# Kernel tuning notes

Hardware: AMD Instinct MI355X
Metric: run time of the kernel (lower is better)

Reference implementation:

```python
import jax, jax.numpy as jnp
import numpy as np

N, E, B = 100000, 1600000, 512
NE, EE, H = 32, 32, 64
SCALE = float(2**48 - 1)


def _mlp2(x, W1, b1, W2, b2):
    # Linear -> ReLU -> Linear
    return jax.nn.relu(x @ W1 + b1) @ W2 + b2


def _gine(x, src, dst, e, W1, b1, W2, b2, n):
    # GINEConv (eps=0): nn(x + sum_j relu(x_j + e_ij))
    m = jax.nn.relu(x[src] + e)                      # [E, d] gather + edge add
    agg = jax.ops.segment_sum(m, dst, num_segments=n)  # scatter-add to targets
    return _mlp2(x + agg, W1, b1, W2, b2)


def _encode(names, edge_index, edge_attr, batch,
            idW1, idb1, idW2, idb2, edW1, edb1, edW2, edb2,
            c1W1, c1b1, c1W2, c1b2, c2W1, c2b1, c2W2, c2b2, linW, linb):
    norm = jnp.clip((names.astype(jnp.float32) + 2.0) / SCALE, 0.0, 1.0)[:, None]
    x = _mlp2(norm, idW1, idb1, idW2, idb2)          # [N, NE]
    e = _mlp2(edge_attr, edW1, edb1, edW2, edb2)     # [E, EE]
    src, dst = edge_index[0], edge_index[1]
    x = jax.nn.relu(_gine(x, src, dst, e, c1W1, c1b1, c1W2, c1b2, N))
    e2 = e @ linW + linb                             # edge lin for conv2 (EE->H)
    x = jax.nn.relu(_gine(x, src, dst, e2, c2W1, c2b1, c2W2, c2b2, N))
    sums = jax.ops.segment_sum(x, batch, num_segments=B)
    cnt = jax.ops.segment_sum(jnp.ones((x.shape[0],), x.dtype), batch, num_segments=B)
    return sums / jnp.maximum(cnt, 1.0)[:, None]     # global_mean_pool


def setup_inputs() -> dict:
    key = jax.random.key(0)
    ks = iter(jax.random.split(key, 64))
    def w(shape):
        return jax.random.normal(next(ks), shape, dtype=jnp.float32) * 0.05
    d = {}
    d['node_names_s'] = jax.random.randint(next(ks), (N,), 0, 1000000)
    d['edge_index_s'] = jax.random.randint(next(ks), (2, E), 0, N)
    d['edge_attr_s'] = jax.random.uniform(next(ks), (E, 1), dtype=jnp.float32)
    d['batch_s'] = jnp.sort(jax.random.randint(next(ks), (N,), 0, B))
    d['node_names_g'] = jax.random.randint(next(ks), (N,), 0, 1000000)
    d['edge_index_g'] = jax.random.randint(next(ks), (2, E), 0, N)
    d['edge_attr_g'] = jax.random.uniform(next(ks), (E, 1), dtype=jnp.float32)
    d['batch_g'] = jnp.sort(jax.random.randint(next(ks), (N,), 0, B))
    d['depth'] = jax.random.uniform(next(ks), (B,), dtype=jnp.float32)
    # shared encoders
    d['idW1'], d['idb1'], d['idW2'], d['idb2'] = w((1, NE)), w((NE,)), w((NE, NE)), w((NE,))
    d['edW1'], d['edb1'], d['edW2'], d['edb2'] = w((1, EE)), w((EE,)), w((EE, EE)), w((EE,))
    # state convs
    d['s1W1'], d['s1b1'], d['s1W2'], d['s1b2'] = w((NE, H)), w((H,)), w((H, H)), w((H,))
    d['s2W1'], d['s2b1'], d['s2W2'], d['s2b2'] = w((H, H)), w((H,)), w((H, H)), w((H,))
    d['s2linW'], d['s2linb'] = w((EE, H)), w((H,))
    # goal convs
    d['g1W1'], d['g1b1'], d['g1W2'], d['g1b2'] = w((NE, H)), w((H,)), w((H, H)), w((H,))
    d['g2W1'], d['g2b1'], d['g2W2'], d['g2b2'] = w((H, H)), w((H,)), w((H, H)), w((H,))
    d['g2linW'], d['g2linb'] = w((EE, H)), w((H,))
    d['rW1'], d['rb1'], d['rW2'], d['rb2'] = w((2 * H + 1, H)), w((H,)), w((H, 1)), w((1,))
    return d


def reference(node_names_s, edge_index_s, edge_attr_s, batch_s,
              node_names_g, edge_index_g, edge_attr_g, batch_g, depth,
              idW1, idb1, idW2, idb2, edW1, edb1, edW2, edb2,
              s1W1, s1b1, s1W2, s1b2, s2W1, s2b1, s2W2, s2b2, s2linW, s2linb,
              g1W1, g1b1, g1W2, g1b2, g2W1, g2b1, g2W2, g2b2, g2linW, g2linb,
              rW1, rb1, rW2, rb2):
    s = _encode(node_names_s, edge_index_s, edge_attr_s, batch_s,
                idW1, idb1, idW2, idb2, edW1, edb1, edW2, edb2,
                s1W1, s1b1, s1W2, s1b2, s2W1, s2b1, s2W2, s2b2, s2linW, s2linb)
    g = _encode(node_names_g, edge_index_g, edge_attr_g, batch_g,
                idW1, idb1, idW2, idb2, edW1, edb1, edW2, edb2,
                g1W1, g1b1, g1W2, g1b2, g2W1, g2b1, g2W2, g2b2, g2linW, g2linb)
    z = jnp.concatenate([s, g, depth[:, None]], axis=1)  # [B, 2H+1]
    return _mlp2(z, rW1, rb1, rW2, rb2)[:, 0]            # [B]
```

## Files before the change

kernel.cpp:

```cpp
#include <hip/hip_runtime.h>
#include <hip/hip_fp16.h>
#include <stdint.h>

namespace {

constexpr int NN   = 100000;
constexpr int TN   = 2 * NN;
constexpr int NEDG = 1600000;
constexpr int TE   = 2 * NEDG;
constexpr int NBAT = 512;
constexpr int NSEG = 33;

constexpr int NC     = 782;
constexpr int TILE   = 4096;
constexpr int ABLK   = (TE + TILE - 1) / TILE;
constexpr int ENTCAP = 5120;

constexpr int CONVBLK = 2048;

constexpr int S1H = 20;
constexpr int S2H = 36;

constexpr int TAB_BP = 0;
constexpr int TAB_D1 = 32;
// ... 103 lines not shown
    if (t < 32) bp[t] = tabs[TAB_BP + t];
    for (int i = t; i < NC; i += 256) hist[i] = 0;
    __syncthreads();
    int base = blockIdx.x * TILE;
#pragma unroll
    for (int j = 0; j < 16; ++j) {
      int i = base + j * 256 + t;
      if (i < TE) {
        int d = (i < NEDG) ? dst_s[i] : (dst_g[i - NEDG] + NN);
        atomicAdd(&hist[d >> 8], 1);
      }
    }
    __syncthreads();
    int loc[4];
    int sum = 0;
#pragma unroll
    for (int j = 0; j < 4; ++j) {
      int b = t * 4 + j;
      int v = (b < NC) ? hist[b] : 0;
      loc[j] = sum; sum += v;
    }
    scanbuf[t] = sum;
    __syncthreads();
    for (int st = 1; st < 256; st <<= 1) {
      int u = (t >= st) ? scanbuf[t - st] : 0;
      __syncthreads();
      scanbuf[t] += u;
      __syncthreads();
    }
    int texcl = scanbuf[t] - sum;
#pragma unroll
    for (int j = 0; j < 4; ++j) {
      int b = t * 4 + j;
      if (b < NC) { lofs[b] = texcl + loc[j]; lcur[b] = 0; }
    }
    __syncthreads();
    for (int b = t; b < NC; b += 256) {
      int c = hist[b];
      hist[b] = c ? atomicAdd(&gcur[b], c) : 0;
    }
    __syncthreads();
#pragma unroll
    for (int j = 0; j < 16; ++j) {
      int i = base + j * 256 + t;
      if (i < TE) {
        int sl, d; float a;
        if (i < NEDG) { sl = src_s[i]; d = dst_s[i]; a = attr_s[i]; }
        else { int k = i - NEDG; sl = src_g[k]; d = dst_g[k] + NN; a = attr_g[k]; }
        int seg = 0;
#pragma unroll
        for (int q = 0; q < 32; ++q) seg += (bp[q] < a);
        int c = d >> 8;
        int r = atomicAdd(&lcur[c], 1);
        int s = lofs[c] + r;
        sorted[s] = make_int2(sl | ((d & 255) << 17) | (seg << 25), __float_as_int(a));
        addr[s] = c * ENTCAP + hist[c] + r;
      }
    }
    __syncthreads();
    int tot = (base + TILE <= TE) ? TILE : (TE - base);
    for (int s = t; s < tot; s += 256) part[addr[s]] = sorted[s];
  } else if (blockIdx.x < ABLK + 782) {
    int n = (blockIdx.x - ABLK) * 256 + t;
    if (n >= TN) return;
    int name = (n < NN) ? names_s[n] : names_g[n - NN];
    float norm = ((float)name + 2.0f) / 281474976710655.0f;
    norm = fminf(fmaxf(norm, 0.0f), 1.0f);
    float h[32];
#pragma unroll
    for (int i = 0; i < 32; ++i) h[i] = relu_(fmaf(norm, idW1[i], idb1[i]));
    int2* outh = (int2*)(x0h + (size_t)n * 32);
    for (int j0 = 0; j0 < 32; j0 += 4) {
      float a0 = idb2[j0], a1 = idb2[j0 + 1], a2 = idb2[j0 + 2], a3 = idb2[j0 + 3];
#pragma unroll
      for (int i = 0; i < 32; ++i) {
        float hv = h[i];
        a0 = fmaf(hv, idW2[i * 32 + j0],     a0);
        a1 = fmaf(hv, idW2[i * 32 + j0 + 1], a1);
        a2 = fmaf(hv, idW2[i * 32 + j0 + 2], a2);
        a3 = fmaf(hv, idW2[i * 32 + j0 + 3], a3);
      }
      outh[j0 >> 2] = make_int2(f2h2(a0, a1), f2h2(a2, a3));
    }
  } else {
    int blk = blockIdx.x - ABLK - 782;
    int half = blk >= 391;
    const int* bat = half ? bat_g : bat_s;
    int* start = half ? start_g : start_s;
    int i = (blk - half * 391) * 256 + t;
    if (i >= NN) return;
    int cur = bat[i];
    int prev = (i == 0) ? -1 : bat[i - 1];
    for (int b = prev + 1; b <= cur; ++b) start[b] = i;
    if (i == NN - 1) {
      for (int b = cur + 1; b <= NBAT; ++b) start[b] = NN;
    }
  }
}

__global__ __launch_bounds__(1024) void coarse_scan(
    const int* __restrict__ gcur, int* __restrict__ cbase, int* __restrict__ rowptr) {
  __shared__ int s[1024];
  int t = threadIdx.x;
  int v = (t < NC) ? min(gcur[t], ENTCAP) : 0;
  s[t] = v;
  __syncthreads();
  for (int st = 1; st < 1024; st <<= 1) {
    int u = (t >= st) ? s[t - st] : 0;
    __syncthreads();
    s[t] += u;
    __syncthreads();
  }
  if (t < NC) cbase[t] = s[t] - v;
  if (t == 0) rowptr[TN] = TE;
}

__global__ __launch_bounds__(256) void partition_to_csr(
    const int* __restrict__ gcur, const int* __restrict__ cbase,
    const int2* __restrict__ part,
    int* __restrict__ rowptr, int2* __restrict__ colattr) {
  __shared__ int2 outE[ENTCAP];
  __shared__ int hist[256];
  __shared__ int cur[256];
  __shared__ int sc[256];
  int t = threadIdx.x, b = blockIdx.x;
  hist[t] = 0;
  __syncthreads();
  int cnt = min(gcur[b], ENTCAP);
  int ibase = b * ENTCAP;
  int obase = cbase[b];
  for (int i = t; i < cnt; i += 256)
    atomicAdd(&hist[(part[ibase + i].x >> 17) & 255], 1);
  __syncthreads();
  int v = hist[t];
  sc[t] = v;
  __syncthreads();
  for (int st = 1; st < 256; st <<= 1) {
    int u = (t >= st) ? sc[t - st] : 0;
    __syncthreads();
    sc[t] += u;
    __syncthreads();
  }
  int excl = sc[t] - v;
  int gnode = b * 256 + t;
  if (gnode < TN) rowptr[gnode] = obase + excl;
  cur[t] = excl;
  __syncthreads();
  for (int i = t; i < cnt; i += 256) {
    int2 e = part[ibase + i];
    int dl = (e.x >> 17) & 255;
    int srcn = e.x & 0x1FFFF;
    int seg = (e.x >> 25) & 63;
    int pos = atomicAdd(&cur[dl], 1);
    outE[pos] = make_int2(srcn | (seg << 20), e.y);
  }
  __syncthreads();
  for (int i = t; i < cnt; i += 256) colattr[obase + i] = outE[i];
}

__global__ __launch_bounds__(256) void conv1_dual(
    const __half* __restrict__ x0h,
    const int* __restrict__ rowptr, const int2* __restrict__ colattr,
    const float* __restrict__ tabs, float* __restrict__ hb) {
  __shared__ __half2 dt2[NSEG * S1H];
  __shared__ __half2 ct2[NSEG * S1H];
  for (int i = threadIdx.x; i < NSEG * 16; i += 256) {
    int s = i >> 4, j = i & 15;
    dt2[s * S1H + j] = __floats2half2_rn(tabs[TAB_D1 + s * 32 + 2 * j],
                                         tabs[TAB_D1 + s * 32 + 2 * j + 1]);
    ct2[s * S1H + j] = __floats2half2_rn(tabs[TAB_C1 + s * 32 + 2 * j],
                                         tabs[TAB_C1 + s * 32 + 2 * j + 1]);
  }
  __syncthreads();
  int lane = threadIdx.x & 63;
  int sub = lane & 7;
  int f0  = (lane >> 3) * 4;
  int h0  = (lane >> 3) * 2;
  int wid = blockIdx.x * 4 + (threadIdx.x >> 6);
  int nb = rowptr[wid], ne = rowptr[wid + 1];
  for (int n = wid; n < TN; n += 4 * CONVBLK) {
    int beg = nb, end = ne;
    int n2 = n + 4 * CONVBLK;
    if (n2 < TN) { nb = rowptr[n2]; ne = rowptr[n2 + 1]; }
    const __half* xb = x0h + (n >= NN ? (size_t)NN * 32 : 0);
    int2 sv = make_int2(0, 0);
    if (sub == 0) sv = *(const int2*)(x0h + (size_t)n * 32 + f0);
    float4 acc = make_float4(0.f, 0.f, 0.f, 0.f);
    for (int k = beg + sub; k < end; k += 16) {
      int2 ca0 = colattr[k];
      int kb = k + 8;
      bool has1 = kb < end;
      int2 ca1 = has1 ? colattr[kb] : ca0;
      unsigned p0 = (unsigned)ca0.x, p1 = (unsigned)ca1.x;
      int s0 = (int)(p0 & 0xFFFFFu), g0 = (int)(p0 >> 20);
      int s1 = (int)(p1 & 0xFFFFFu), g1 = (int)(p1 >> 20);
      float a0 = __int_as_float(ca0.y), a1 = __int_as_float(ca1.y);
      __half2 az0 = __floats2half2_rn(a0, a0);
      __half2 az1 = __floats2half2_rn(a1, a1);
      int2 xv0 = *(const int2*)(xb + (size_t)s0 * 32 + f0);
      int2 xv1 = *(const int2*)(xb + (size_t)s1 * 32 + f0);
      int2 dv0 = *(const int2*)&dt2[g0 * S1H + h0];
      int2 cv0 = *(const int2*)&ct2[g0 * S1H + h0];
      __half2 v;
      float2 f;
      v = __hadd2(bch(xv0.x), __hfma2(az0, bch(dv0.x), bch(cv0.x)));
      f = __half22float2(v); acc.x += relu_(f.x); acc.y += relu_(f.y);
      v = __hadd2(bch(xv0.y), __hfma2(az0, bch(dv0.y), bch(cv0.y)));
      f = __half22float2(v); acc.z += relu_(f.x); acc.w += relu_(f.y);
      if (has1) {
        int2 dv1 = *(const int2*)&dt2[g1 * S1H + h0];
        int2 cv1 = *(const int2*)&ct2[g1 * S1H + h0];
        v = __hadd2(bch(xv1.x), __hfma2(az1, bch(dv1.x), bch(cv1.x)));
        f = __half22float2(v); acc.x += relu_(f.x); acc.y += relu_(f.y);
        v = __hadd2(bch(xv1.y), __hfma2(az1, bch(dv1.y), bch(cv1.y)));
        f = __half22float2(v); acc.z += relu_(f.x); acc.w += relu_(f.y);
      }
    }
#pragma unroll
    for (int m = 1; m < 8; m <<= 1) {
      float4 o = shfl_xor4(acc, m);
      acc.x += o.x; acc.y += o.y; acc.z += o.z; acc.w += o.w;
    }
    if (sub == 0) {
      float2 t0 = __half22float2(bch(sv.x)), t1 = __half22float2(bch(sv.y));
      *(float4*)(hb + (size_t)n * 32 + f0) =
          make_float4(t0.x + acc.x, t0.y + acc.y, t1.x + acc.z, t1.y + acc.w);
    }
  }
}

__global__ __launch_bounds__(256) void conv2_dual(
    const __half* __restrict__ x1h,
    const int* __restrict__ rowptr, const int2* __restrict__ colattr,
    const float* __restrict__ tabs, float* __restrict__ hb) {
  __shared__ __half2 dt2[NSEG * S2H];
  __shared__ __half2 ct2[NSEG * S2H];
  int halfg = blockIdx.x >= (CONVBLK / 2);
  const float* d2 = tabs + TAB_E2 + (size_t)halfg * 2 * NSEG * 64;
  for (int i = threadIdx.x; i < NSEG * 32; i += 256) {
    int s = i >> 5, j = i & 31;
    dt2[s * S2H + j] = __floats2half2_rn(d2[s * 64 + 2 * j], d2[s * 64 + 2 * j + 1]);
    ct2[s * S2H + j] = __floats2half2_rn(d2[NSEG * 64 + s * 64 + 2 * j],
                                         d2[NSEG * 64 + s * 64 + 2 * j + 1]);
  }
  __syncthreads();
  const __half* xb = x1h + (size_t)halfg * NN * 64;
  int lane = threadIdx.x & 63;
  int sub = lane & 7;
  int f0  = (lane >> 3) * 8;
  int h0  = (lane >> 3) * 4;
  int wid = (blockIdx.x - halfg * (CONVBLK / 2)) * 4 + (threadIdx.x >> 6);
  int nlim = halfg * NN + NN;
  int n0 = halfg * NN + wid;
  int nb = rowptr[n0], ne = rowptr[n0 + 1];
  for (int n = n0; n < nlim; n += 2 * CONVBLK) {
    int beg = nb, end = ne;
    int n2 = n + 2 * CONVBLK;
    if (n2 < nlim) { nb = rowptr[n2]; ne = rowptr[n2 + 1]; }
    int4 sv0 = make_int4(0, 0, 0, 0);
    if (sub == 0) sv0 = *(const int4*)(x1h + (size_t)n * 64 + f0);
    float4 accA = make_float4(0.f, 0.f, 0.f, 0.f);
    float4 accB = make_float4(0.f, 0.f, 0.f, 0.f);
    for (int k = beg + sub; k < end; k += 16) {
      int2 ca0 = colattr[k];
      int kb = k + 8;
      bool has1 = kb < end;
      int2 ca1 = has1 ? colattr[kb] : ca0;
      unsigned p0 = (unsigned)ca0.x, p1 = (unsigned)ca1.x;
      int s0 = (int)(p0 & 0xFFFFFu), g0 = (int)(p0 >> 20);
      int s1 = (int)(p1 & 0xFFFFFu), g1 = (int)(p1 >> 20);
      float a0 = __int_as_float(ca0.y), a1 = __int_as_float(ca1.y);
      __half2 az0 = __floats2half2_rn(a0, a0);
      __half2 az1 = __floats2half2_rn(a1, a1);
      int4 xv0 = *(const int4*)(xb + (size_t)s0 * 64 + f0);
      int4 xv1 = *(const int4*)(xb + (size_t)s1 * 64 + f0);
      int4 dv0 = *(const int4*)&dt2[g0 * S2H + h0];
      int4 cv0 = *(const int4*)&ct2[g0 * S2H + h0];
      __half2 v;
      float2 f;
      v = __hadd2(bch(xv0.x), __hfma2(az0, bch(dv0.x), bch(cv0.x)));
      f = __half22float2(v); accA.x += relu_(f.x); accA.y += relu_(f.y);
      v = __hadd2(bch(xv0.y), __hfma2(az0, bch(dv0.y), bch(cv0.y)));
      f = __half22float2(v); accA.z += relu_(f.x); accA.w += relu_(f.y);
      v = __hadd2(bch(xv0.z), __hfma2(az0, bch(dv0.z), bch(cv0.z)));
      f = __half22float2(v); accB.x += relu_(f.x); accB.y += relu_(f.y);
      v = __hadd2(bch(xv0.w), __hfma2(az0, bch(dv0.w), bch(cv0.w)));
      f = __half22float2(v); accB.z += relu_(f.x); accB.w += relu_(f.y);
      if (has1) {
        int4 dv1 = *(const int4*)&dt2[g1 * S2H + h0];
        int4 cv1 = *(const int4*)&ct2[g1 * S2H + h0];
        v = __hadd2(bch(xv1.x), __hfma2(az1, bch(dv1.x), bch(cv1.x)));
        f = __half22float2(v); accA.x += relu_(f.x); accA.y += relu_(f.y);
        v = __hadd2(bch(xv1.y), __hfma2(az1, bch(dv1.y), bch(cv1.y)));
        f = __half22float2(v); accA.z += relu_(f.x); accA.w += relu_(f.y);
        v = __hadd2(bch(xv1.z), __hfma2(az1, bch(dv1.z), bch(cv1.z)));
        f = __half22float2(v); accB.x += relu_(f.x); accB.y += relu_(f.y);
        v = __hadd2(bch(xv1.w), __hfma2(az1, bch(dv1.w), bch(cv1.w)));
        f = __half22float2(v); accB.z += relu_(f.x); accB.w += relu_(f.y);
      }
    }
#pragma unroll
    for (int m = 1; m < 8; m <<= 1) {
      float4 oA = shfl_xor4(accA, m);
      float4 oB = shfl_xor4(accB, m);
      accA.x += oA.x; accA.y += oA.y; accA.z += oA.z; accA.w += oA.w;
      accB.x += oB.x; accB.y += oB.y; accB.z += oB.z; accB.w += oB.w;
    }
    if (sub == 0) {
      float2 t0 = __half22float2(bch(sv0.x)), t1 = __half22float2(bch(sv0.y));
      float2 t2 = __half22float2(bch(sv0.z)), t3 = __half22float2(bch(sv0.w));
      float* op = hb + (size_t)n * 64 + f0;
      *(float4*)op       = make_float4(t0.x + accA.x, t0.y + accA.y, t1.x + accA.z, t1.y + accA.w);
      *(float4*)(op + 4) = make_float4(t2.x + accB.x, t2.y + accB.y, t3.x + accB.z, t3.y + accB.w);
    }
  }
}

__global__ __launch_bounds__(256) void mlp1_dual(
    const float* __restrict__ hin,
    const float* __restrict__ sW1, const float* __restrict__ sb1,
    const float* __restrict__ sW2, const float* __restrict__ sb2,
    const float* __restrict__ gW1, const float* __restrict__ gb1,
    const float* __restrict__ gW2, const float* __restrict__ gb2,
    __half* __restrict__ hout) {
  constexpr int IN = 32;
  __shared__ float hsT[IN][65];
  __shared__ float ysT[64][65];
  int base = blockIdx.x * 64;
  for (int idx = threadIdx.x; idx < 64 * IN; idx += 256) {
    int node = idx / IN, k = idx - node * IN;
    hsT[k][node] = hin[(size_t)(base + node) * IN + k];
  }
  __syncthreads();
  int nt = threadIdx.x >> 4, jx = threadIdx.x & 15;
  int n0 = nt * 4, f0 = jx * 4;
  bool isg = (base + n0) >= NN;
  const float* W1 = isg ? gW1 : sW1;
  const float* b1 = isg ? gb1 : sb1;
  const float* W2 = isg ? gW2 : sW2;
  const float* b2 = isg ? gb2 : sb2;
  float4 acc0, acc1, acc2, acc3;
  {
    const float4 b = *(const float4*)(b1 + f0);
    acc0 = b; acc1 = b; acc2 = b; acc3 = b;
  }
  for (int k = 0; k < IN; ++k) {
    const float4 h = *(const float4*)&hsT[k][n0];
    const float4 w = *(const float4*)(W1 + k * 64 + f0);
    acc0.x = fmaf(h.x, w.x, acc0.x); acc0.y = fmaf(h.x, w.y, acc0.y);
    acc0.z = fmaf(h.x, w.z, acc0.z); acc0.w = fmaf(h.x, w.w, acc0.w);
    acc1.x = fmaf(h.y, w.x, acc1.x); acc1.y = fmaf(h.y, w.y, acc1.y);
    acc1.z = fmaf(h.y, w.z, acc1.z); acc1.w = fmaf(h.y, w.w, acc1.w);
    acc2.x = fmaf(h.z, w.x, acc2.x); acc2.y = fmaf(h.z, w.y, acc2.y);
    acc2.z = fmaf(h.z, w.z, acc2.z); acc2.w = fmaf(h.z, w.w, acc2.w);
    acc3.x = fmaf(h.w, w.x, acc3.x); acc3.y = fmaf(h.w, w.y, acc3.y);
    acc3.z = fmaf(h.w, w.z, acc3.z); acc3.w = fmaf(h.w, w.w, acc3.w);
  }
  ysT[f0 + 0][n0 + 0] = relu_(acc0.x); ysT[f0 + 1][n0 + 0] = relu_(acc0.y);
  ysT[f0 + 2][n0 + 0] = relu_(acc0.z); ysT[f0 + 3][n0 + 0] = relu_(acc0.w);
  ysT[f0 + 0][n0 + 1] = relu_(acc1.x); ysT[f0 + 1][n0 + 1] = relu_(acc1.y);
  ysT[f0 + 2][n0 + 1] = relu_(acc1.z); ysT[f0 + 3][n0 + 1] = relu_(acc1.w);
  ysT[f0 + 0][n0 + 2] = relu_(acc2.x); ysT[f0 + 1][n0 + 2] = relu_(acc2.y);
  ysT[f0 + 2][n0 + 2] = relu_(acc2.z); ysT[f0 + 3][n0 + 2] = relu_(acc2.w);
  ysT[f0 + 0][n0 + 3] = relu_(acc3.x); ysT[f0 + 1][n0 + 3] = relu_(acc3.y);
  ysT[f0 + 2][n0 + 3] = relu_(acc3.z); ysT[f0 + 3][n0 + 3] = relu_(acc3.w);
  __syncthreads();
  {
    const float4 b = *(const float4*)(b2 + f0);
    acc0 = b; acc1 = b; acc2 = b; acc3 = b;
  }
  for (int k = 0; k < 64; ++k) {
    const float4 h = *(const float4*)&ysT[k][n0];
    const float4 w = *(const float4*)(W2 + k * 64 + f0);
    acc0.x = fmaf(h.x, w.x, acc0.x); acc0.y = fmaf(h.x, w.y, acc0.y);
    acc0.z = fmaf(h.x, w.z, acc0.z); acc0.w = fmaf(h.x, w.w, acc0.w);
    acc1.x = fmaf(h.y, w.x, acc1.x); acc1.y = fmaf(h.y, w.y, acc1.y);
    acc1.z = fmaf(h.y, w.z, acc1.z); acc1.w = fmaf(h.y, w.w, acc1.w);
    acc2.x = fmaf(h.z, w.x, acc2.x); acc2.y = fmaf(h.z, w.y, acc2.y);
    acc2.z = fmaf(h.z, w.z, acc2.z); acc2.w = fmaf(h.z, w.w, acc2.w);
    acc3.x = fmaf(h.w, w.x, acc3.x); acc3.y = fmaf(h.w, w.y, acc3.y);
    acc3.z = fmaf(h.w, w.z, acc3.z); acc3.w = fmaf(h.w, w.w, acc3.w);
  }
  float4 o;
  o = make_float4(relu_(acc0.x), relu_(acc0.y), relu_(acc0.z), relu_(acc0.w));
  *(int2*)(hout + (size_t)(base + n0 + 0) * 64 + f0) = make_int2(f2h2(o.x, o.y), f2h2(o.z, o.w));
  o = make_float4(relu_(acc1.x), relu_(acc1.y), relu_(acc1.z), relu_(acc1.w));
  *(int2*)(hout + (size_t)(base + n0 + 1) * 64 + f0) = make_int2(f2h2(o.x, o.y), f2h2(o.z, o.w));
  o = make_float4(relu_(acc2.x), relu_(acc2.y), relu_(acc2.z), relu_(acc2.w));
  *(int2*)(hout + (size_t)(base + n0 + 2) * 64 + f0) = make_int2(f2h2(o.x, o.y), f2h2(o.z, o.w));
  o = make_float4(relu_(acc3.x), relu_(acc3.y), relu_(acc3.z), relu_(acc3.w));
  *(int2*)(hout + (size_t)(base + n0 + 3) * 64 + f0) = make_int2(f2h2(o.x, o.y), f2h2(o.z, o.w));
}

__global__ __launch_bounds__(256) void mlp2_pool_dual(
    const float* __restrict__ hin,
    const float* __restrict__ sW1, const float* __restrict__ sb1,
    const float* __restrict__ sW2, const float* __restrict__ sb2,
    const float* __restrict__ gW1, const float* __restrict__ gb1,
    const float* __restrict__ gW2, const float* __restrict__ gb2,
    const int* __restrict__ bat_s, const int* __restrict__ bat_g,
    float* __restrict__ psum) {
  constexpr int IN = 64;
  __shared__ float hsT[IN][65];
  __shared__ float ysT[64][65];
  __shared__ int pid[64];
  int base = blockIdx.x * 64;
  for (int idx = threadIdx.x; idx < 64 * IN; idx += 256) {
    int node = idx / IN, k = idx - node * IN;
    hsT[k][node] = hin[(size_t)(base + node) * IN + k];
  }
  if (threadIdx.x < 64) {
    int gb = base + threadIdx.x;
    pid[threadIdx.x] = (gb < NN) ? bat_s[gb] : (NBAT + bat_g[gb - NN]);
  }
  __syncthreads();
  int nt = threadIdx.x >> 4, jx = threadIdx.x & 15;
  int n0 = nt * 4, f0 = jx * 4;
  bool isg = (base + n0) >= NN;
  const float* W1 = isg ? gW1 : sW1;
  const float* b1 = isg ? gb1 : sb1;
  const float* W2 = isg ? gW2 : sW2;
  const float* b2 = isg ? gb2 : sb2;
  float4 acc0, acc1, acc2, acc3;
  {
    const float4 b = *(const float4*)(b1 + f0);
    acc0 = b; acc1 = b; acc2 = b; acc3 = b;
  }
  for (int k = 0; k < IN; ++k) {
    const float4 h = *(const float4*)&hsT[k][n0];
    const float4 w = *(const float4*)(W1 + k * 64 + f0);
    acc0.x = fmaf(h.x, w.x, acc0.x); acc0.y = fmaf(h.x, w.y, acc0.y);
    acc0.z = fmaf(h.x, w.z, acc0.z); acc0.w = fmaf(h.x, w.w, acc0.w);
    acc1.x = fmaf(h.y, w.x, acc1.x); acc1.y = fmaf(h.y, w.y, acc1.y);
    acc1.z = fmaf(h.y, w.z, acc1.z); acc1.w = fmaf(h.y, w.w, acc1.w);
    acc2.x = fmaf(h.z, w.x, acc2.x); acc2.y = fmaf(h.z, w.y, acc2.y);
    acc2.z = fmaf(h.z, w.z, acc2.z); acc2.w = fmaf(h.z, w.w, acc2.w);
    acc3.x = fmaf(h.w, w.x, acc3.x); acc3.y = fmaf(h.w, w.y, acc3.y);
    acc3.z = fmaf(h.w, w.z, acc3.z); acc3.w = fmaf(h.w, w.w, acc3.w);
  }
  ysT[f0 + 0][n0 + 0] = relu_(acc0.x); ysT[f0 + 1][n0 + 0] = relu_(acc0.y);
  ysT[f0 + 2][n0 + 0] = relu_(acc0.z); ysT[f0 + 3][n0 + 0] = relu_(acc0.w);
  ysT[f0 + 0][n0 + 1] = relu_(acc1.x); ysT[f0 + 1][n0 + 1] = relu_(acc1.y);
  ysT[f0 + 2][n0 + 1] = relu_(acc1.z); ysT[f0 + 3][n0 + 1] = relu_(acc1.w);
  ysT[f0 + 0][n0 + 2] = relu_(acc2.x); ysT[f0 + 1][n0 + 2] = relu_(acc2.y);
  ysT[f0 + 2][n0 + 2] = relu_(acc2.z); ysT[f0 + 3][n0 + 2] = relu_(acc2.w);
  ysT[f0 + 0][n0 + 3] = relu_(acc3.x); ysT[f0 + 1][n0 + 3] = relu_(acc3.y);
  ysT[f0 + 2][n0 + 3] = relu_(acc3.z); ysT[f0 + 3][n0 + 3] = relu_(acc3.w);
  __syncthreads();
  {
    const float4 b = *(const float4*)(b2 + f0);
    acc0 = b; acc1 = b; acc2 = b; acc3 = b;
  }
  for (int k = 0; k < 64; ++k) {
    const float4 h = *(const float4*)&ysT[k][n0];
    const float4 w = *(const float4*)(W2 + k * 64 + f0);
    acc0.x = fmaf(h.x, w.x, acc0.x); acc0.y = fmaf(h.x, w.y, acc0.y);
    acc0.z = fmaf(h.x, w.z, acc0.z); acc0.w = fmaf(h.x, w.w, acc0.w);
    acc1.x = fmaf(h.y, w.x, acc1.x); acc1.y = fmaf(h.y, w.y, acc1.y);
    acc1.z = fmaf(h.y, w.z, acc1.z); acc1.w = fmaf(h.y, w.w, acc1.w);
    acc2.x = fmaf(h.z, w.x, acc2.x); acc2.y = fmaf(h.z, w.y, acc2.y);
    acc2.z = fmaf(h.z, w.z, acc2.z); acc2.w = fmaf(h.z, w.w, acc2.w);
    acc3.x = fmaf(h.w, w.x, acc3.x); acc3.y = fmaf(h.w, w.y, acc3.y);
    acc3.z = fmaf(h.w, w.z, acc3.z); acc3.w = fmaf(h.w, w.w, acc3.w);
  }
  __syncthreads();
  ysT[f0 + 0][n0 + 0] = relu_(acc0.x); ysT[f0 + 1][n0 + 0] = relu_(acc0.y);
  ysT[f0 + 2][n0 + 0] = relu_(acc0.z); ysT[f0 + 3][n0 + 0] = relu_(acc0.w);
// ... 147 lines not shown
```

Baseline: 569.7 us.

## Process two nodes per wave with masked branchless edge loops in GINE convs

Each wave in conv1 and conv2 now handles two destination nodes at a time. A single masked, branch-free loop issues four colattr loads and four gathered x loads per iteration, which raises memory-level parallelism for the latency-bound gathers. Out-of-range lanes use clamped indices with a zero multiplier instead of a branch. The CSR build also pre-converts the edge attribute to a packed half2, removing a conversion per edge. The cost is extra register pressure and wasted loads when the two nodes have unequal degrees.

```diff
diff --git a/kernel.cpp b/kernel.cpp
--- a/kernel.cpp
+++ b/kernel.cpp
@@ -279,10 +279,23 @@
     int srcn = e.x & 0x1FFFF;
     int seg = (e.x >> 25) & 63;
     int pos = atomicAdd(&cur[dl], 1);
-    outE[pos] = make_int2(srcn | (seg << 20), e.y);
+    float af = __int_as_float(e.y);
+    outE[pos] = make_int2(srcn | (seg << 20), f2h2(af, af));
   }
   __syncthreads();
   for (int i = t; i < cnt; i += 256) colattr[obase + i] = outE[i];
+}
+
+__device__ __forceinline__ void e1m(int2 xv, unsigned p, int h0, __half2 az, float m,
+                                    const __half2* dt2, const __half2* ct2, float4& A) {
+  int g = (int)(p >> 20);
+  int2 dv = *(const int2*)&dt2[g * S1H + h0];
+  int2 cv = *(const int2*)&ct2[g * S1H + h0];
+  __half2 v; float2 f;
+  v = __hadd2(bch(xv.x), __hfma2(az, bch(dv.x), bch(cv.x)));
+  f = __half22float2(v); A.x = fmaf(m, relu_(f.x), A.x); A.y = fmaf(m, relu_(f.y), A.y);
+  v = __hadd2(bch(xv.y), __hfma2(az, bch(dv.y), bch(cv.y)));
+  f = __half22float2(v); A.z = fmaf(m, relu_(f.x), A.z); A.w = fmaf(m, relu_(f.y), A.w);
 }
 
 __global__ __launch_bounds__(256) void conv1_dual(
@@ -303,57 +316,87 @@
   int sub = lane & 7;
   int f0  = (lane >> 3) * 4;
   int h0  = (lane >> 3) * 2;
+  constexpr int STR = 4 * CONVBLK;
   int wid = blockIdx.x * 4 + (threadIdx.x >> 6);
-  int nb = rowptr[wid], ne = rowptr[wid + 1];
-  for (int n = wid; n < TN; n += 4 * CONVBLK) {
-    int beg = nb, end = ne;
-    int n2 = n + 4 * CONVBLK;
-    if (n2 < TN) { nb = rowptr[n2]; ne = rowptr[n2 + 1]; }
-    const __half* xb = x0h + (n >= NN ? (size_t)NN * 32 : 0);
-    int2 sv = make_int2(0, 0);
-    if (sub == 0) sv = *(const int2*)(x0h + (size_t)n * 32 + f0);
-    float4 acc = make_float4(0.f, 0.f, 0.f, 0.f);
-    for (int k = beg + sub; k < end; k += 16) {
-      int2 ca0 = colattr[k];
-      int kb = k + 8;
-      bool has1 = kb < end;
-      int2 ca1 = has1 ? colattr[kb] : ca0;
-      unsigned p0 = (unsigned)ca0.x, p1 = (unsigned)ca1.x;
-      int s0 = (int)(p0 & 0xFFFFFu), g0 = (int)(p0 >> 20);
-      int s1 = (int)(p1 & 0xFFFFFu), g1 = (int)(p1 >> 20);
-      float a0 = __int_as_float(ca0.y), a1 = __int_as_float(ca1.y);
-      __half2 az0 = __floats2half2_rn(a0, a0);
-      __half2 az1 = __floats2half2_rn(a1, a1);
-      int2 xv0 = *(const int2*)(xb + (size_t)s0 * 32 + f0);
-      int2 xv1 = *(const int2*)(xb + (size_t)s1 * 32 + f0);
-      int2 dv0 = *(const int2*)&dt2[g0 * S1H + h0];
-      int2 cv0 = *(const int2*)&ct2[g0 * S1H + h0];
-      __half2 v;
-      float2 f;
-      v = __hadd2(bch(xv0.x), __hfma2(az0, bch(dv0.x), bch(cv0.x)));
-      f = __half22float2(v); acc.x += relu_(f.x); acc.y += relu_(f.y);
-      v = __hadd2(bch(xv0.y), __hfma2(az0, bch(dv0.y), bch(cv0.y)));
-      f = __half22float2(v); acc.z += relu_(f.x); acc.w += relu_(f.y);
-      if (has1) {
-        int2 dv1 = *(const int2*)&dt2[g1 * S1H + h0];
-        int2 cv1 = *(const int2*)&ct2[g1 * S1H + h0];
-        v = __hadd2(bch(xv1.x), __hfma2(az1, bch(dv1.x), bch(cv1.x)));
-        f = __half22float2(v); acc.x += relu_(f.x); acc.y += relu_(f.y);
-        v = __hadd2(bch(xv1.y), __hfma2(az1, bch(dv1.y), bch(cv1.y)));
-        f = __half22float2(v); acc.z += relu_(f.x); acc.w += relu_(f.y);
+  int nbA = rowptr[wid], neA = rowptr[wid + 1];
+  int nbB = 0, neB = 0;
+  if (wid + STR < TN) { nbB = rowptr[wid + STR]; neB = rowptr[wid + STR + 1]; }
+  for (int n = wid; n < TN; n += 2 * STR) {
+    int nB = n + STR;
+    bool hasB = nB < TN;
+    int begA = nbA, endA = neA, begB = nbB, endB = neB;
+    int nn = n + 2 * STR;
+    if (nn < TN) {
+      nbA = rowptr[nn]; neA = rowptr[nn + 1];
+      if (nn + STR < TN) { nbB = rowptr[nn + STR]; neB = rowptr[nn + STR + 1]; }
+      else { nbB = 0; neB = 0; }
+    }
+    const __half* xbA = x0h + (n  >= NN ? (size_t)NN * 32 : 0);
+    const __half* xbB = x0h + (nB >= NN ? (size_t)NN * 32 : 0);
+    float4 accA = make_float4(0.f, 0.f, 0.f, 0.f);
+    float4 accB = make_float4(0.f, 0.f, 0.f, 0.f);
+    int kA = begA + sub, kB = begB + sub;
+    while (__any((kA < endA) || (kB < endB))) {
+      int iA0 = min(kA, TE - 1), iA1 = min(kA + 8, TE - 1);
+      int iB0 = min(kB, TE - 1), iB1 = min(kB + 8, TE - 1);
+      float mA0 = (kA < endA)     ? 1.f : 0.f;
+      float mA1 = (kA + 8 < endA) ? 1.f : 0.f;
+      float mB0 = (kB < endB)     ? 1.f : 0.f;
+      float mB1 = (kB + 8 < endB) ? 1.f : 0.f;
+      int2 cA0 = colattr[iA0], cA1 = colattr[iA1];
+      int2 cB0 = colattr[iB0], cB1 = colattr[iB1];
+      unsigned pA0 = (unsigned)cA0.x, pA1 = (unsigned)cA1.x;
+      unsigned pB0 = (unsigned)cB0.x, pB1 = (unsigned)cB1.x;
+      int2 xA0 = *(const int2*)(xbA + (size_t)(pA0 & 0xFFFFFu) * 32 + f0);
+      int2 xA1 = *(const int2*)(xbA + (size_t)(pA1 & 0xFFFFFu) * 32 + f0);
+      int2 xB0 = *(const int2*)(xbB + (size_t)(pB0 & 0xFFFFFu) * 32 + f0);
+      int2 xB1 = *(const int2*)(xbB + (size_t)(pB1 & 0xFFFFFu) * 32 + f0);
+      e1m(xA0, pA0, h0, bch(cA0.y), mA0, dt2, ct2, accA);
+      e1m(xA1, pA1, h0, bch(cA1.y), mA1, dt2, ct2, accA);
+      e1m(xB0, pB0, h0, bch(cB0.y), mB0, dt2, ct2, accB);
+      e1m(xB1, pB1, h0, bch(cB1.y), mB1, dt2, ct2, accB);
+      kA += 16; kB += 16;
+    }
+    int2 svA = make_int2(0, 0), svB = make_int2(0, 0);
+    if (sub == 0) {
+      svA = *(const int2*)(x0h + (size_t)n * 32 + f0);
+      if (hasB) svB = *(const int2*)(x0h + (size_t)nB * 32 + f0);
+    }
+#pragma unroll
+    for (int m = 1; m < 8; m <<= 1) {
+      float4 oA = shfl_xor4(accA, m);
+      float4 oB = shfl_xor4(accB, m);
+      accA.x += oA.x; accA.y += oA.y; accA.z += oA.z; accA.w += oA.w;
+      accB.x += oB.x; accB.y += oB.y; accB.z += oB.z; accB.w += oB.w;
+    }
+    if (sub == 0) {
+      float2 t0 = __half22float2(bch(svA.x)), t1 = __half22float2(bch(svA.y));
+      *(float4*)(hb + (size_t)n * 32 + f0) =
+          make_float4(t0.x + accA.x, t0.y + accA.y, t1.x + accA.z, t1.y + accA.w);
+      if (hasB) {
+        float2 u0 = __half22float2(bch(svB.x)), u1 = __half22float2(bch(svB.y));
+        *(float4*)(hb + (size_t)nB * 32 + f0) =
+            make_float4(u0.x + accB.x, u0.y + accB.y, u1.x + accB.z, u1.y + accB.w);
       }
     }
-#pragma unroll
-    for (int m = 1; m < 8; m <<= 1) {
-      float4 o = shfl_xor4(acc, m);
-      acc.x += o.x; acc.y += o.y; acc.z += o.z; acc.w += o.w;
-    }
-    if (sub == 0) {
-      float2 t0 = __half22float2(bch(sv.x)), t1 = __half22float2(bch(sv.y));
-      *(float4*)(hb + (size_t)n * 32 + f0) =
-          make_float4(t0.x + acc.x, t0.y + acc.y, t1.x + acc.z, t1.y + acc.w);
-    }
-  }
+  }
+}
+
+__device__ __forceinline__ void e2m(int4 xv, unsigned p, int h0, __half2 az, float m,
+                                    const __half2* dt2, const __half2* ct2,
+                                    float4& A, float4& B) {
+  int g = (int)(p >> 20);
+  int4 dv = *(const int4*)&dt2[g * S2H + h0];
+  int4 cv = *(const int4*)&ct2[g * S2H + h0];
+  __half2 v; float2 f;
+  v = __hadd2(bch(xv.x), __hfma2(az, bch(dv.x), bch(cv.x)));
+  f = __half22float2(v); A.x = fmaf(m, relu_(f.x), A.x); A.y = fmaf(m, relu_(f.y), A.y);
+  v = __hadd2(bch(xv.y), __hfma2(az, bch(dv.y), bch(cv.y)));
+  f = __half22float2(v); A.z = fmaf(m, relu_(f.x), A.z); A.w = fmaf(m, relu_(f.y), A.w);
+  v = __hadd2(bch(xv.z), __hfma2(az, bch(dv.z), bch(cv.z)));
+  f = __half22float2(v); B.x = fmaf(m, relu_(f.x), B.x); B.y = fmaf(m, relu_(f.y), B.y);
+  v = __hadd2(bch(xv.w), __hfma2(az, bch(dv.w), bch(cv.w)));
+  f = __half22float2(v); B.z = fmaf(m, relu_(f.x), B.z); B.w = fmaf(m, relu_(f.y), B.w);
 }
 
 __global__ __launch_bounds__(256) void conv2_dual(
@@ -376,69 +419,78 @@
   int sub = lane & 7;
   int f0  = (lane >> 3) * 8;
   int h0  = (lane >> 3) * 4;
+  constexpr int STR2 = 2 * CONVBLK;
   int wid = (blockIdx.x - halfg * (CONVBLK / 2)) * 4 + (threadIdx.x >> 6);
   int nlim = halfg * NN + NN;
   int n0 = halfg * NN + wid;
-  int nb = rowptr[n0], ne = rowptr[n0 + 1];
-  for (int n = n0; n < nlim; n += 2 * CONVBLK) {
-    int beg = nb, end = ne;
-    int n2 = n + 2 * CONVBLK;
-    if (n2 < nlim) { nb = rowptr[n2]; ne = rowptr[n2 + 1]; }
-    int4 sv0 = make_int4(0, 0, 0, 0);
-    if (sub == 0) sv0 = *(const int4*)(x1h + (size_t)n * 64 + f0);
-    float4 accA = make_float4(0.f, 0.f, 0.f, 0.f);
-    float4 accB = make_float4(0.f, 0.f, 0.f, 0.f);
-    for (int k = beg + sub; k < end; k += 16) {
-      int2 ca0 = colattr[k];
-      int kb = k + 8;
-      bool has1 = kb < end;
-      int2 ca1 = has1 ? colattr[kb] : ca0;
-      unsigned p0 = (unsigned)ca0.x, p1 = (unsigned)ca1.x;
-      int s0 = (int)(p0 & 0xFFFFFu), g0 = (int)(p0 >> 20);
-      int s1 = (int)(p1 & 0xFFFFFu), g1 = (int)(p1 >> 20);
-      float a0 = __int_as_float(ca0.y), a1 = __int_as_float(ca1.y);
-      __half2 az0 = __floats2half2_rn(a0, a0);
-      __half2 az1 = __floats2half2_rn(a1, a1);
-      int4 xv0 = *(const int4*)(xb + (size_t)s0 * 64 + f0);
-      int4 xv1 = *(const int4*)(xb + (size_t)s1 * 64 + f0);
-      int4 dv0 = *(const int4*)&dt2[g0 * S2H + h0];
-      int4 cv0 = *(const int4*)&ct2[g0 * S2H + h0];
-      __half2 v;
-      float2 f;
-      v = __hadd2(bch(xv0.x), __hfma2(az0, bch(dv0.x), bch(cv0.x)));
-      f = __half22float2(v); accA.x += relu_(f.x); accA.y += relu_(f.y);
-      v = __hadd2(bch(xv0.y), __hfma2(az0, bch(dv0.y), bch(cv0.y)));
-      f = __half22float2(v); accA.z += relu_(f.x); accA.w += relu_(f.y);
-      v = __hadd2(bch(xv0.z), __hfma2(az0, bch(dv0.z), bch(cv0.z)));
-      f = __half22float2(v); accB.x += relu_(f.x); accB.y += relu_(f.y);
-      v = __hadd2(bch(xv0.w), __hfma2(az0, bch(dv0.w), bch(cv0.w)));
-      f = __half22float2(v); accB.z += relu_(f.x); accB.w += relu_(f.y);
-      if (has1) {
-        int4 dv1 = *(const int4*)&dt2[g1 * S2H + h0];
-        int4 cv1 = *(const int4*)&ct2[g1 * S2H + h0];
-        v = __hadd2(bch(xv1.x), __hfma2(az1, bch(dv1.x), bch(cv1.x)));
-        f = __half22float2(v); accA.x += relu_(f.x); accA.y += relu_(f.y);
-        v = __hadd2(bch(xv1.y), __hfma2(az1, bch(dv1.y), bch(cv1.y)));
-        f = __half22float2(v); accA.z += relu_(f.x); accA.w += relu_(f.y);
-        v = __hadd2(bch(xv1.z), __hfma2(az1, bch(dv1.z), bch(cv1.z)));
-        f = __half22float2(v); accB.x += relu_(f.x); accB.y += relu_(f.y);
-        v = __hadd2(bch(xv1.w), __hfma2(az1, bch(dv1.w), bch(cv1.w)));
-        f = __half22float2(v); accB.z += relu_(f.x); accB.w += relu_(f.y);
+  int nbA = rowptr[n0], neA = rowptr[n0 + 1];
+  int nbB = 0, neB = 0;
+  if (n0 + STR2 < nlim) { nbB = rowptr[n0 + STR2]; neB = rowptr[n0 + STR2 + 1]; }
+  for (int n = n0; n < nlim; n += 2 * STR2) {
+    int nB = n + STR2;
+    bool hasB = nB < nlim;
+    int begA = nbA, endA = neA, begB = nbB, endB = neB;
+    int nn = n + 2 * STR2;
+    if (nn < nlim) {
+      nbA = rowptr[nn]; neA = rowptr[nn + 1];
+      if (nn + STR2 < nlim) { nbB = rowptr[nn + STR2]; neB = rowptr[nn + STR2 + 1]; }
+      else { nbB = 0; neB = 0; }
+    }
+    float4 accA0 = make_float4(0.f, 0.f, 0.f, 0.f);
+    float4 accA1 = make_float4(0.f, 0.f, 0.f, 0.f);
+    float4 accB0 = make_float4(0.f, 0.f, 0.f, 0.f);
+    float4 accB1 = make_float4(0.f, 0.f, 0.f, 0.f);
+    int kA = begA + sub, kB = begB + sub;
+    while (__any((kA < endA) || (kB < endB))) {
+      int iA0 = min(kA, TE - 1), iA1 = min(kA + 8, TE - 1);
+      int iB0 = min(kB, TE - 1), iB1 = min(kB + 8, TE - 1);
+      float mA0 = (kA < endA)     ? 1.f : 0.f;
+      float mA1 = (kA + 8 < endA) ? 1.f : 0.f;
+      float mB0 = (kB < endB)     ? 1.f : 0.f;
+      float mB1 = (kB + 8 < endB) ? 1.f : 0.f;
+      int2 cA0 = colattr[iA0], cA1 = colattr[iA1];
+      int2 cB0 = colattr[iB0], cB1 = colattr[iB1];
+      unsigned pA0 = (unsigned)cA0.x, pA1 = (unsigned)cA1.x;
+      unsigned pB0 = (unsigned)cB0.x, pB1 = (unsigned)cB1.x;
+      int4 xA0 = *(const int4*)(xb + (size_t)(pA0 & 0xFFFFFu) * 64 + f0);
+      int4 xA1 = *(const int4*)(xb + (size_t)(pA1 & 0xFFFFFu) * 64 + f0);
+      int4 xB0 = *(const int4*)(xb + (size_t)(pB0 & 0xFFFFFu) * 64 + f0);
+      int4 xB1 = *(const int4*)(xb + (size_t)(pB1 & 0xFFFFFu) * 64 + f0);
+      e2m(xA0, pA0, h0, bch(cA0.y), mA0, dt2, ct2, accA0, accA1);
+      e2m(xA1, pA1, h0, bch(cA1.y), mA1, dt2, ct2, accA0, accA1);
+      e2m(xB0, pB0, h0, bch(cB0.y), mB0, dt2, ct2, accB0, accB1);
+      e2m(xB1, pB1, h0, bch(cB1.y), mB1, dt2, ct2, accB0, accB1);
+      kA += 16; kB += 16;
+    }
+    int4 svA = make_int4(0, 0, 0, 0), svB = make_int4(0, 0, 0, 0);
+    if (sub == 0) {
+      svA = *(const int4*)(x1h + (size_t)n * 64 + f0);
+      if (hasB) svB = *(const int4*)(x1h + (size_t)nB * 64 + f0);
+    }
+#pragma unroll
+    for (int m = 1; m < 8; m <<= 1) {
+      float4 o0 = shfl_xor4(accA0, m);
+      float4 o1 = shfl_xor4(accA1, m);
+      float4 o2 = shfl_xor4(accB0, m);
+      float4 o3 = shfl_xor4(accB1, m);
+      accA0.x += o0.x; accA0.y += o0.y; accA0.z += o0.z; accA0.w += o0.w;
+      accA1.x += o1.x; accA1.y += o1.y; accA1.z += o1.z; accA1.w += o1.w;
+      accB0.x += o2.x; accB0.y += o2.y; accB0.z += o2.z; accB0.w += o2.w;
+      accB1.x += o3.x; accB1.y += o3.y; accB1.z += o3.z; accB1.w += o3.w;
+    }
+    if (sub == 0) {
+      float2 t0 = __half22float2(bch(svA.x)), t1 = __half22float2(bch(svA.y));
+      float2 t2 = __half22float2(bch(svA.z)), t3 = __half22float2(bch(svA.w));
+      float* op = hb + (size_t)n * 64 + f0;
+      *(float4*)op       = make_float4(t0.x + accA0.x, t0.y + accA0.y, t1.x + accA0.z, t1.y + accA0.w);
+      *(float4*)(op + 4) = make_float4(t2.x + accA1.x, t2.y + accA1.y, t3.x + accA1.z, t3.y + accA1.w);
+      if (hasB) {
+        float2 u0 = __half22float2(bch(svB.x)), u1 = __half22float2(bch(svB.y));
+        float2 u2 = __half22float2(bch(svB.z)), u3 = __half22float2(bch(svB.w));
+        float* op2 = hb + (size_t)nB * 64 + f0;
+        *(float4*)op2       = make_float4(u0.x + accB0.x, u0.y + accB0.y, u1.x + accB0.z, u1.y + accB0.w);
+        *(float4*)(op2 + 4) = make_float4(u2.x + accB1.x, u2.y + accB1.y, u3.x + accB1.z, u3.y + accB1.w);
       }
-    }
-#pragma unroll
-    for (int m = 1; m < 8; m <<= 1) {
-      float4 oA = shfl_xor4(accA, m);
-      float4 oB = shfl_xor4(accB, m);
-      accA.x += oA.x; accA.y += oA.y; accA.z += oA.z; accA.w += oA.w;
-      accB.x += oB.x; accB.y += oB.y; accB.z += oB.z; accB.w += oB.w;
-    }
-    if (sub == 0) {
-      float2 t0 = __half22float2(bch(sv0.x)), t1 = __half22float2(bch(sv0.y));
-      float2 t2 = __half22float2(bch(sv0.z)), t3 = __half22float2(bch(sv0.w));
-      float* op = hb + (size_t)n * 64 + f0;
-      *(float4*)op       = make_float4(t0.x + accA.x, t0.y + accA.y, t1.x + accA.z, t1.y + accA.w);
-      *(float4*)(op + 4) = make_float4(t2.x + accB.x, t2.y + accB.y, t3.x + accB.z, t3.y + accB.w);
     }
   }
 }
```

Result: slower. 637.9 us (+12.0%).

## Prefetch next node's edge records and use branchless masked edge accumulation

Applied to the files above, without the earlier changes.

The two conv gather kernels now preload the first two colattr entries of the next node while processing the current node, so the first dependent load chain is overlapped. The inner loop becomes branchless: indices are clamped, out-of-range edges get a zero multiplier, and accumulation uses fmaf. The CSR build stores the edge attribute pre-converted to a packed half2, which removes per-edge float-to-half conversions. The cost is extra masked gathers for the padding slots of short rows, plus some added register pressure.

```diff
diff --git a/kernel.cpp b/kernel.cpp
--- a/kernel.cpp
+++ b/kernel.cpp
@@ -279,10 +279,23 @@
     int srcn = e.x & 0x1FFFF;
     int seg = (e.x >> 25) & 63;
     int pos = atomicAdd(&cur[dl], 1);
-    outE[pos] = make_int2(srcn | (seg << 20), e.y);
+    float af = __int_as_float(e.y);
+    outE[pos] = make_int2(srcn | (seg << 20), f2h2(af, af));
   }
   __syncthreads();
   for (int i = t; i < cnt; i += 256) colattr[obase + i] = outE[i];
+}
+
+__device__ __forceinline__ void e1m(int2 xv, unsigned p, int h0, __half2 az, float m,
+                                    const __half2* dt2, const __half2* ct2, float4& A) {
+  int g = (int)(p >> 20);
+  int2 dv = *(const int2*)&dt2[g * S1H + h0];
+  int2 cv = *(const int2*)&ct2[g * S1H + h0];
+  __half2 v; float2 f;
+  v = __hadd2(bch(xv.x), __hfma2(az, bch(dv.x), bch(cv.x)));
+  f = __half22float2(v); A.x = fmaf(m, relu_(f.x), A.x); A.y = fmaf(m, relu_(f.y), A.y);
+  v = __hadd2(bch(xv.y), __hfma2(az, bch(dv.y), bch(cv.y)));
+  f = __half22float2(v); A.z = fmaf(m, relu_(f.x), A.z); A.w = fmaf(m, relu_(f.y), A.w);
 }
 
 __global__ __launch_bounds__(256) void conv1_dual(
@@ -303,45 +316,43 @@
   int sub = lane & 7;
   int f0  = (lane >> 3) * 4;
   int h0  = (lane >> 3) * 2;
-  int wid = blockIdx.x * 4 + (threadIdx.x >> 6);
-  int nb = rowptr[wid], ne = rowptr[wid + 1];
-  for (int n = wid; n < TN; n += 4 * CONVBLK) {
-    int beg = nb, end = ne;
-    int n2 = n + 4 * CONVBLK;
-    if (n2 < TN) { nb = rowptr[n2]; ne = rowptr[n2 + 1]; }
+  constexpr int STR = 4 * CONVBLK;
+  int n = blockIdx.x * 4 + (threadIdx.x >> 6);
+  int begC = rowptr[n], endC = rowptr[n + 1];
+  int2 c0 = colattr[min(begC + sub, TE - 1)];
+  int2 c1 = colattr[min(begC + sub + 8, TE - 1)];
+  for (; n < TN; n += STR) {
+    int nn = n + STR;
+    int begN = 0, endN = 0;
+    if (nn < TN) { begN = rowptr[nn]; endN = rowptr[nn + 1]; }
     const __half* xb = x0h + (n >= NN ? (size_t)NN * 32 : 0);
     int2 sv = make_int2(0, 0);
     if (sub == 0) sv = *(const int2*)(x0h + (size_t)n * 32 + f0);
     float4 acc = make_float4(0.f, 0.f, 0.f, 0.f);
-    for (int k = beg + sub; k < end; k += 16) {
-      int2 ca0 = colattr[k];
-      int kb = k + 8;
-      bool has1 = kb < end;
-      int2 ca1 = has1 ? colattr[kb] : ca0;
-      unsigned p0 = (unsigned)ca0.x, p1 = (unsigned)ca1.x;
-      int s0 = (int)(p0 & 0xFFFFFu), g0 = (int)(p0 >> 20);
-      int s1 = (int)(p1 & 0xFFFFFu), g1 = (int)(p1 >> 20);
-      float a0 = __int_as_float(ca0.y), a1 = __int_as_float(ca1.y);
-      __half2 az0 = __floats2half2_rn(a0, a0);
-      __half2 az1 = __floats2half2_rn(a1, a1);
-      int2 xv0 = *(const int2*)(xb + (size_t)s0 * 32 + f0);
-      int2 xv1 = *(const int2*)(xb + (size_t)s1 * 32 + f0);
-      int2 dv0 = *(const int2*)&dt2[g0 * S1H + h0];
-      int2 cv0 = *(const int2*)&ct2[g0 * S1H + h0];
-      __half2 v;
-      float2 f;
-      v = __hadd2(bch(xv0.x), __hfma2(az0, bch(dv0.x), bch(cv0.x)));
-      f = __half22float2(v); acc.x += relu_(f.x); acc.y += relu_(f.y);
-      v = __hadd2(bch(xv0.y), __hfma2(az0, bch(dv0.y), bch(cv0.y)));
-      f = __half22float2(v); acc.z += relu_(f.x); acc.w += relu_(f.y);
-      if (has1) {
-        int2 dv1 = *(const int2*)&dt2[g1 * S1H + h0];
-        int2 cv1 = *(const int2*)&ct2[g1 * S1H + h0];
-        v = __hadd2(bch(xv1.x), __hfma2(az1, bch(dv1.x), bch(cv1.x)));
-        f = __half22float2(v); acc.x += relu_(f.x); acc.y += relu_(f.y);
-        v = __hadd2(bch(xv1.y), __hfma2(az1, bch(dv1.y), bch(cv1.y)));
-        f = __half22float2(v); acc.z += relu_(f.x); acc.w += relu_(f.y);
-      }
+    int k0 = begC + sub;
+    int2 cN0, cN1;
+    {
+      float m0 = (k0 < endC) ? 1.f : 0.f;
+      float m1 = (k0 + 8 < endC) ? 1.f : 0.f;
+      unsigned p0 = (unsigned)c0.x, p1 = (unsigned)c1.x;
+      int2 xv0 = *(const int2*)(xb + (size_t)(p0 & 0xFFFFFu) * 32 + f0);
+      int2 xv1 = *(const int2*)(xb + (size_t)(p1 & 0xFFFFFu) * 32 + f0);
+      cN0 = colattr[min(begN + sub, TE - 1)];
+      cN1 = colattr[min(begN + sub + 8, TE - 1)];
+      e1m(xv0, p0, h0, bch(c0.y), m0, dt2, ct2, acc);
+      e1m(xv1, p1, h0, bch(c1.y), m1, dt2, ct2, acc);
+    }
+    for (int kb = begC + 16; kb < endC; kb += 16) {
+      int k = kb + sub;
+      float m0 = (k < endC) ? 1.f : 0.f;
+      float m1 = (k + 8 < endC) ? 1.f : 0.f;
+      int2 d0 = colattr[min(k, TE - 1)];
+      int2 d1 = colattr[min(k + 8, TE - 1)];
+      unsigned p0 = (unsigned)d0.x, p1 = (unsigned)d1.x;
+      int2 xv0 = *(const int2*)(xb + (size_t)(p0 & 0xFFFFFu) * 32 + f0);
+      int2 xv1 = *(const int2*)(xb + (size_t)(p1 & 0xFFFFFu) * 32 + f0);
+      e1m(xv0, p0, h0, bch(d0.y), m0, dt2, ct2, acc);
+      e1m(xv1, p1, h0, bch(d1.y), m1, dt2, ct2, acc);
     }
 #pragma unroll
     for (int m = 1; m < 8; m <<= 1) {
@@ -353,7 +364,26 @@
       *(float4*)(hb + (size_t)n * 32 + f0) =
           make_float4(t0.x + acc.x, t0.y + acc.y, t1.x + acc.z, t1.y + acc.w);
     }
-  }
+    c0 = cN0; c1 = cN1;
+    begC = begN; endC = endN;
+  }
+}
+
+__device__ __forceinline__ void e2m(int4 xv, unsigned p, int h0, __half2 az, float m,
+                                    const __half2* dt2, const __half2* ct2,
+                                    float4& A, float4& B) {
+  int g = (int)(p >> 20);
+  int4 dv = *(const int4*)&dt2[g * S2H + h0];
+  int4 cv = *(const int4*)&ct2[g * S2H + h0];
+  __half2 v; float2 f;
+  v = __hadd2(bch(xv.x), __hfma2(az, bch(dv.x), bch(cv.x)));
+  f = __half22float2(v); A.x = fmaf(m, relu_(f.x), A.x); A.y = fmaf(m, relu_(f.y), A.y);
+  v = __hadd2(bch(xv.y), __hfma2(az, bch(dv.y), bch(cv.y)));
+  f = __half22float2(v); A.z = fmaf(m, relu_(f.x), A.z); A.w = fmaf(m, relu_(f.y), A.w);
+  v = __hadd2(bch(xv.z), __hfma2(az, bch(dv.z), bch(cv.z)));
+  f = __half22float2(v); B.x = fmaf(m, relu_(f.x), B.x); B.y = fmaf(m, relu_(f.y), B.y);
+  v = __hadd2(bch(xv.w), __hfma2(az, bch(dv.w), bch(cv.w)));
+  f = __half22float2(v); B.z = fmaf(m, relu_(f.x), B.z); B.w = fmaf(m, relu_(f.y), B.w);
 }
 
 __global__ __launch_bounds__(256) void conv2_dual(
@@ -376,55 +406,45 @@
   int sub = lane & 7;
   int f0  = (lane >> 3) * 8;
   int h0  = (lane >> 3) * 4;
+  constexpr int STR2 = 2 * CONVBLK;
   int wid = (blockIdx.x - halfg * (CONVBLK / 2)) * 4 + (threadIdx.x >> 6);
   int nlim = halfg * NN + NN;
-  int n0 = halfg * NN + wid;
-  int nb = rowptr[n0], ne = rowptr[n0 + 1];
-  for (int n = n0; n < nlim; n += 2 * CONVBLK) {
-    int beg = nb, end = ne;
-    int n2 = n + 2 * CONVBLK;
-    if (n2 < nlim) { nb = rowptr[n2]; ne = rowptr[n2 + 1]; }
-    int4 sv0 = make_int4(0, 0, 0, 0);
-    if (sub == 0) sv0 = *(const int4*)(x1h + (size_t)n * 64 + f0);
+  int n = halfg * NN + wid;
+  int begC = rowptr[n], endC = rowptr[n + 1];
+  int2 c0 = colattr[min(begC + sub, TE - 1)];
+  int2 c1 = colattr[min(begC + sub + 8, TE - 1)];
+  for (; n < nlim; n += STR2) {
+    int nn = n + STR2;
+    int begN = 0, endN = 0;
+    if (nn < nlim) { begN = rowptr[nn]; endN = rowptr[nn + 1]; }
+    int4 sv = make_int4(0, 0, 0, 0);
+    if (sub == 0) sv = *(const int4*)(x1h + (size_t)n * 64 + f0);
     float4 accA = make_float4(0.f, 0.f, 0.f, 0.f);
     float4 accB = make_float4(0.f, 0.f, 0.f, 0.f);
-    for (int k = beg + sub; k < end; k += 16) {
-      int2 ca0 = colattr[k];
-      int kb = k + 8;
-      bool has1 = kb < end;
-      int2 ca1 = has1 ? colattr[kb] : ca0;
-      unsigned p0 = (unsigned)ca0.x, p1 = (unsigned)ca1.x;
-      int s0 = (int)(p0 & 0xFFFFFu), g0 = (int)(p0 >> 20);
-      int s1 = (int)(p1 & 0xFFFFFu), g1 = (int)(p1 >> 20);
-      float a0 = __int_as_float(ca0.y), a1 = __int_as_float(ca1.y);
-      __half2 az0 = __floats2half2_rn(a0, a0);
-      __half2 az1 = __floats2half2_rn(a1, a1);
-      int4 xv0 = *(const int4*)(xb + (size_t)s0 * 64 + f0);
-      int4 xv1 = *(const int4*)(xb + (size_t)s1 * 64 + f0);
-      int4 dv0 = *(const int4*)&dt2[g0 * S2H + h0];
-      int4 cv0 = *(const int4*)&ct2[g0 * S2H + h0];
-      __half2 v;
-      float2 f;
-      v = __hadd2(bch(xv0.x), __hfma2(az0, bch(dv0.x), bch(cv0.x)));
-      f = __half22float2(v); accA.x += relu_(f.x); accA.y += relu_(f.y);
-      v = __hadd2(bch(xv0.y), __hfma2(az0, bch(dv0.y), bch(cv0.y)));
-      f = __half22float2(v); accA.z += relu_(f.x); accA.w += relu_(f.y);
-      v = __hadd2(bch(xv0.z), __hfma2(az0, bch(dv0.z), bch(cv0.z)));
-      f = __half22float2(v); accB.x += relu_(f.x); accB.y += relu_(f.y);
-      v = __hadd2(bch(xv0.w), __hfma2(az0, bch(dv0.w), bch(cv0.w)));
-      f = __half22float2(v); accB.z += relu_(f.x); accB.w += relu_(f.y);
-      if (has1) {
-        int4 dv1 = *(const int4*)&dt2[g1 * S2H + h0];
-        int4 cv1 = *(const int4*)&ct2[g1 * S2H + h0];
-        v = __hadd2(bch(xv1.x), __hfma2(az1, bch(dv1.x), bch(cv1.x)));
-        f = __half22float2(v); accA.x += relu_(f.x); accA.y += relu_(f.y);
-        v = __hadd2(bch(xv1.y), __hfma2(az1, bch(dv1.y), bch(cv1.y)));
-        f = __half22float2(v); accA.z += relu_(f.x); accA.w += relu_(f.y);
-        v = __hadd2(bch(xv1.z), __hfma2(az1, bch(dv1.z), bch(cv1.z)));
-        f = __half22float2(v); accB.x += relu_(f.x); accB.y += relu_(f.y);
-        v = __hadd2(bch(xv1.w), __hfma2(az1, bch(dv1.w), bch(cv1.w)));
-        f = __half22float2(v); accB.z += relu_(f.x); accB.w += relu_(f.y);
-      }
+    int k0 = begC + sub;
+    int2 cN0, cN1;
+    {
+      float m0 = (k0 < endC) ? 1.f : 0.f;
+      float m1 = (k0 + 8 < endC) ? 1.f : 0.f;
+      unsigned p0 = (unsigned)c0.x, p1 = (unsigned)c1.x;
+      int4 xv0 = *(const int4*)(xb + (size_t)(p0 & 0xFFFFFu) * 64 + f0);
+      int4 xv1 = *(const int4*)(xb + (size_t)(p1 & 0xFFFFFu) * 64 + f0);
+      cN0 = colattr[min(begN + sub, TE - 1)];
+      cN1 = colattr[min(begN + sub + 8, TE - 1)];
+      e2m(xv0, p0, h0, bch(c0.y), m0, dt2, ct2, accA, accB);
+      e2m(xv1, p1, h0, bch(c1.y), m1, dt2, ct2, accA, accB);
+    }
+    for (int kb = begC + 16; kb < endC; kb += 16) {
+      int k = kb + sub;
+      float m0 = (k < endC) ? 1.f : 0.f;
+      float m1 = (k + 8 < endC) ? 1.f : 0.f;
+      int2 d0 = colattr[min(k, TE - 1)];
+      int2 d1 = colattr[min(k + 8, TE - 1)];
+      unsigned p0 = (unsigned)d0.x, p1 = (unsigned)d1.x;
+      int4 xv0 = *(const int4*)(xb + (size_t)(p0 & 0xFFFFFu) * 64 + f0);
+      int4 xv1 = *(const int4*)(xb + (size_t)(p1 & 0xFFFFFu) * 64 + f0);
+      e2m(xv0, p0, h0, bch(d0.y), m0, dt2, ct2, accA, accB);
+      e2m(xv1, p1, h0, bch(d1.y), m1, dt2, ct2, accA, accB);
     }
 #pragma unroll
     for (int m = 1; m < 8; m <<= 1) {
@@ -434,12 +454,14 @@
       accB.x += oB.x; accB.y += oB.y; accB.z += oB.z; accB.w += oB.w;
     }
     if (sub == 0) {
-      float2 t0 = __half22float2(bch(sv0.x)), t1 = __half22float2(bch(sv0.y));
-      float2 t2 = __half22float2(bch(sv0.z)), t3 = __half22float2(bch(sv0.w));
+      float2 t0 = __half22float2(bch(sv.x)), t1 = __half22float2(bch(sv.y));
+      float2 t2 = __half22float2(bch(sv.z)), t3 = __half22float2(bch(sv.w));
       float* op = hb + (size_t)n * 64 + f0;
       *(float4*)op       = make_float4(t0.x + accA.x, t0.y + accA.y, t1.x + accA.z, t1.y + accA.w);
       *(float4*)(op + 4) = make_float4(t2.x + accB.x, t2.y + accB.y, t3.x + accB.z, t3.y + accB.w);
     }
+    c0 = cN0; c1 = cN1;
+    begC = begN; endC = endN;
   }
 }
 
```

Result: slower. 629.8 us (+10.6%).
